# Performance work log

Hardware: AMD Instinct MI355X
Metric: run time of the kernel (lower is better)

The kernel has to match this reference:

```python
import jax, jax.numpy as jnp
import numpy as np

DIM = 1024
NUM_HEADS = 16
HEAD_DIM = DIM // NUM_HEADS
SEQ = 2048
BATCH = 2


def setup_inputs() -> dict:
    key = jax.random.key(0)
    kx, kq, kk, kv, ko, kb = jax.random.split(key, 6)
    s = 0.02
    return {
        "x": jax.random.normal(kx, (BATCH, SEQ, DIM), dtype=jnp.float32),
        "W_q": jax.random.normal(kq, (DIM, DIM), dtype=jnp.float32) * s,
        "W_k": jax.random.normal(kk, (DIM, DIM), dtype=jnp.float32) * s,
        "W_v": jax.random.normal(kv, (DIM, DIM), dtype=jnp.float32) * s,
        "W_o": jax.random.normal(ko, (DIM, DIM), dtype=jnp.float32) * s,
        "b_o": jax.random.normal(kb, (DIM,), dtype=jnp.float32) * s,
    }


def reference(x, W_q, W_k, W_v, W_o, b_o):
    b, n, d = x.shape
    # Linear layers (torch Linear: y = x @ W.T); weights here stored as [out, in]
    q = jnp.einsum('bnd,ed->bne', x, W_q).reshape(b, n, NUM_HEADS, HEAD_DIM)
    k = jnp.einsum('bnd,ed->bne', x, W_k).reshape(b, n, NUM_HEADS, HEAD_DIM)
    v = jnp.einsum('bnd,ed->bne', x, W_v).reshape(b, n, NUM_HEADS, HEAD_DIM)
    # scores: [b, h, q, k]
    scores = jnp.einsum('bqhd,bkhd->bhqk', q, k)
    causal = jnp.tril(jnp.ones((n, n), dtype=bool))  # True = keep
    scores = jnp.where(causal, scores, -jnp.inf)
    weights = jax.nn.softmax(scores / jnp.sqrt(jnp.float32(HEAD_DIM)), axis=-1)
    ctx = jnp.einsum('bhqk,bkhd->bqhd', weights, v).reshape(b, n, d)
    return jnp.einsum('bnd,ed->bne', ctx, W_o) + b_o
```

## Files before the change

### kernel.cpp

```cpp
#include <hip/hip_runtime.h>
#include <hip/hip_bf16.h>

#define DIM 1024
#define NHEADS 16
#define HD 64
#define SEQ 2048
#define BATCH 2
#define MROWS (BATCH * SEQ)
#define MB (1024u * 1024u)
#define NT (SEQ / 64)

typedef __bf16 bf16x8 __attribute__((ext_vector_type(8)));
typedef float f32x4 __attribute__((ext_vector_type(4)));
typedef short short8 __attribute__((ext_vector_type(8)));

#define SCQ (0.125f * 1.44269504f)

__device__ __forceinline__ unsigned short f2bf(float f) {
    union { float f; unsigned u; } v; v.f = f;
    unsigned r = v.u + 0x7fffu + ((v.u >> 16) & 1u);
    return (unsigned short)(r >> 16);
}
__device__ __forceinline__ unsigned cvtpk(float lo, float hi) {
    unsigned r;
    asm("v_cvt_pk_bf16_f32 %0, %1, %2" : "=v"(r) : "v"(lo), "v"(hi));
    return r;
}

__device__ __forceinline__ void gld16(const unsigned short* g, unsigned short* l) {
    __builtin_amdgcn_global_load_lds(
        (const __attribute__((address_space(1))) void*)g,
        (__attribute__((address_space(3))) void*)l, 16, 0, 0);
}

#define VWAIT(n) asm volatile("s_waitcnt vmcnt(" #n ")" ::: "memory")
#define BARRIER  do { __builtin_amdgcn_s_barrier(); __builtin_amdgcn_sched_barrier(0); } while (0)

__global__ __launch_bounds__(256) void f2b_kernel(const float* __restrict__ in,
                                                  unsigned short* __restrict__ out,
                                                  int n4) {
    int i = blockIdx.x * 256 + threadIdx.x;
    if (i < n4) {
        float4 v = ((const float4*)in)[i];
        ushort4 o;
        o.x = f2bf(v.x); o.y = f2bf(v.y); o.z = f2bf(v.z); o.w = f2bf(v.w);
        ((ushort4*)out)[i] = o;
    }
}

__global__ __launch_bounds__(256) void f2bw_kernel(
    const float* __restrict__ w0, const float* __restrict__ w1,
    const float* __restrict__ w2, const float* __restrict__ w3,
    unsigned short* __restrict__ o0, unsigned short* __restrict__ o1,
    unsigned short* __restrict__ o2, unsigned short* __restrict__ o3,
    int n4) {
    const float* in; unsigned short* out;
    switch (blockIdx.y) {
        case 0: in = w0; out = o0; break;
        case 1: in = w1; out = o1; break;
        case 2: in = w2; out = o2; break;
        default: in = w3; out = o3; break;
    }
    int i = blockIdx.x * 256 + threadIdx.x;
    if (i < n4) {
        float4 v = ((const float4*)in)[i];
        ushort4 o;
        o.x = f2bf(v.x); o.y = f2bf(v.y); o.z = f2bf(v.z); o.w = f2bf(v.w);
        ((ushort4*)out)[i] = o;
    }
}


#define GEMM_VARS(Aptr, Bptr)                                                  \
    __shared__ unsigned short As[3][128 * 32];                                 \
    __shared__ unsigned short Bs[3][128 * 32];                                 \
    const int tid  = threadIdx.x;                                              \
    const int lane = tid & 63;                                                 \
    const int wid  = tid >> 6;                                                 \
    const int wrow = wid >> 1, wcol = wid & 1;                                 \
    const int l15  = lane & 15;                                                \
    const int lhi  = lane >> 4;                                                \
    f32x4 acc[4][4] = {};                                                      \
    const int r0s = tid >> 2;                                                  \
    const int c0s = (tid & 3) ^ ((r0s >> 1) & 3);                              \
    const int r1s = (tid + 256) >> 2;                                          \
    const int c1s = (tid & 3) ^ ((r1s >> 1) & 3);                              \
    const unsigned short* gA0 = (Aptr) + (size_t)(row0 + r0s) * DIM + c0s * 8; \
    const unsigned short* gA1 = (Aptr) + (size_t)(row0 + r1s) * DIM + c1s * 8; \
    const unsigned short* gB0 = (Bptr) + (size_t)(col0 + r0s) * DIM + c0s * 8; \
    const unsigned short* gB1 = (Bptr) + (size_t)(col0 + r1s) * DIM + c1s * 8;

#define GEMM_STAGE(bi, kofs)                                                   \
    gld16(gA0 + (kofs), &As[bi][tid * 8]);                                     \
    gld16(gA1 + (kofs), &As[bi][(tid + 256) * 8]);                             \
    gld16(gB0 + (kofs), &Bs[bi][tid * 8]);                                     \
    gld16(gB1 + (kofs), &Bs[bi][(tid + 256) * 8]);

#define GEMM_COMPUTE(bi)                                                       \
    {   const unsigned short* Ac = &As[bi][0];                                 \
        const unsigned short* Bc = &Bs[bi][0];                                 \
        bf16x8 af[4], bfr[4];                                                  \
        _Pragma("unroll")                                                      \
        for (int m = 0; m < 4; m++) {                                          \
            int r = wrow * 64 + m * 16 + l15;                                  \
            int c = lhi ^ ((r >> 1) & 3);                                      \
            af[m] = *(const bf16x8*)&Ac[r * 32 + c * 8];                       \
        }                                                                      \
        _Pragma("unroll")                                                      \
        for (int n = 0; n < 4; n++) {                                          \
            int r = wcol * 64 + n * 16 + l15;                                  \
            int c = lhi ^ ((r >> 1) & 3);                                      \
            bfr[n] = *(const bf16x8*)&Bc[r * 32 + c * 8];                      \
        }                                                                      \
        __builtin_amdgcn_s_setprio(1);                                         \
        _Pragma("unroll")                                                      \
        for (int m = 0; m < 4; m++)                                            \
            _Pragma("unroll")                                                  \
            for (int n = 0; n < 4; n++)                                        \
                acc[m][n] = __builtin_amdgcn_mfma_f32_16x16x32_bf16(           \
                    af[m], bfr[n], acc[m][n], 0, 0, 0);                        \
        __builtin_amdgcn_s_setprio(0);                                         \
    }

#define GEMM_PIPELINE()                                                        \
    GEMM_STAGE(0, 0)                                                           \
    GEMM_STAGE(1, 32)                                                          \
    int bi = 0;                                                                \
    for (int k0 = 0; k0 + 96 <= DIM; k0 += 32) {                               \
        VWAIT(4);                                                              \
        BARRIER;                                                               \
        int b2 = bi + 2; if (b2 >= 3) b2 -= 3;                                 \
        GEMM_STAGE(b2, k0 + 64)                                                \
        GEMM_COMPUTE(bi)                                                       \
        bi = (bi + 1 == 3) ? 0 : bi + 1;                                       \
    }                                                                          \
    VWAIT(4);                                                                  \
    BARRIER;                                                                   \
    GEMM_COMPUTE(bi)                                                           \
    bi = (bi + 1 == 3) ? 0 : bi + 1;                                           \
    VWAIT(0);                                                                  \
    BARRIER;                                                                   \
    GEMM_COMPUTE(bi)

__global__ __launch_bounds__(256) void qkv_gemm(
    const unsigned short* __restrict__ A,
    const unsigned short* __restrict__ Wqb,
    const unsigned short* __restrict__ Wkb,
    const unsigned short* __restrict__ Wvb,
    unsigned short* __restrict__ Qb,
    unsigned short* __restrict__ Kbf,
    unsigned short* __restrict__ Vtb)
{
    const int lb  = ((int)blockIdx.x & 7) * 96 + ((int)blockIdx.x >> 3);
    const int xx  = lb % 24;
    const int yy  = lb / 24;
    const int sel = xx >> 3;
    const unsigned short* Bw = (sel == 0) ? Wqb : ((sel == 1) ? Wkb : Wvb);
    const int row0 = yy * 128;
    const int col0 = (xx & 7) * 128;

    GEMM_VARS(A, Bw)
    GEMM_PIPELINE()

    const int cr = lhi * 4;
    unsigned short* outRM = (sel == 0) ? Qb : Kbf;
    #pragma unroll
    for (int m = 0; m < 4; m++) {
        #pragma unroll
        for (int n = 0; n < 4; n++) {
            #pragma unroll
            for (int j = 0; j < 4; j++) {
                int gr = row0 + wrow * 64 + m * 16 + cr + j;
                int gc = col0 + wcol * 64 + n * 16 + l15;
                float v = acc[m][n][j];
                if (sel == 0) v *= SCQ;
                unsigned short hv = f2bf(v);
                if (sel < 2) {
                    outRM[(size_t)gr * DIM + gc] = hv;
                } else {
                    int bb = gr >> 11, s = gr & 2047;
                    int hh = gc >> 6,  d = gc & 63;
                    Vtb[(((size_t)bb * NHEADS + hh) * HD + d) * SEQ + s] = hv;
                }
            }
        }
    }
}

__global__ __launch_bounds__(256) void o_gemm(
    const unsigned short* __restrict__ A,
    const unsigned short* __restrict__ Bw,
    float* __restrict__ Cp,
    const float* __restrict__ bias)
{
    const int lb  = ((int)blockIdx.x & 7) * 32 + ((int)blockIdx.x >> 3);
    const int xx  = lb % 8;
    const int yy  = lb / 8;
    const int row0 = yy * 128;
    const int col0 = xx * 128;

    GEMM_VARS(A, Bw)
    GEMM_PIPELINE()

    const int cr = lhi * 4;
    #pragma unroll
    for (int m = 0; m < 4; m++) {
        #pragma unroll
        for (int n = 0; n < 4; n++) {
            #pragma unroll
            for (int j = 0; j < 4; j++) {
                int gr = row0 + wrow * 64 + m * 16 + cr + j;
                int gc = col0 + wcol * 64 + n * 16 + l15;
                Cp[(size_t)gr * DIM + gc] = acc[m][n][j] + bias[gc];
            }
        }
    }
}

#define ATTN_COMPUTE(bi, t)                                                    \
    {   const unsigned short* Kc = &Ks[bi][0];                                 \
        const unsigned short* Vc = &Vs[bi][0];                                 \
        f32x4 sacc[4] = {};                                                    \
        __builtin_amdgcn_s_setprio(1);                                         \
        _Pragma("unroll")                                                      \
        for (int ks = 0; ks < 2; ++ks) {                                       \
            bf16x8 bq = ks ? aq1 : aq0;                                        \
            _Pragma("unroll")                                                  \
            for (int nt = 0; nt < 4; nt++) {                                   \
                int r = nt * 16 + l15;                                         \
                int c = (ks * 4 + lhi) ^ (r & 7);                              \
                bf16x8 ak = *(const bf16x8*)&Kc[r * 64 + c * 8];               \
                sacc[nt] = __builtin_amdgcn_mfma_f32_16x16x32_bf16(            \
                    ak, bq, sacc[nt], 0, 0, 0);                                \
            }                                                                  \
        }                                                                      \
        __builtin_amdgcn_s_setprio(0);                                         \
        const bool diag = ((t) == qblk);                                       \
        _Pragma("unroll")                                                      \
        for (int nt = 0; nt < 4; nt++) {                                       \
            float pv[4];                                                       \
            _Pragma("unroll")                                                  \
            for (int j = 0; j < 4; j++) {                                      \
                bool msk = diag && (nt * 16 + lhi * 4 + j > (w & 3) * 16 + l15); \
                pv[j] = msk ? 0.f : exp2f(sacc[nt][j]);                        \
            }                                                                  \
            *(uint2*)&Ps[w][l15][nt * 16 + lhi * 4] =                          \
                make_uint2(cvtpk(pv[0], pv[1]), cvtpk(pv[2], pv[3]));          \
        }                                                                      \
        __builtin_amdgcn_s_setprio(1);                                         \
        _Pragma("unroll")                                                      \
        for (int ks = 0; ks < 2; ++ks) {                                       \
            bf16x8 ap = *(const bf16x8*)&Ps[w][l15][ks * 32 + lhi * 8];        \
            _Pragma("unroll")                                                  \
            for (int dt = 0; dt < 4; dt++) {                                   \
                int r = dt * 16 + l15;                                         \
                int c = (ks * 4 + lhi) ^ (r & 7);                              \
                bf16x8 bv = *(const bf16x8*)&Vc[r * 64 + c * 8];               \
                octx[dt] = __builtin_amdgcn_mfma_f32_16x16x32_bf16(            \
                    ap, bv, octx[dt], 0, 0, 0);                                \
            }                                                                  \
            octxS = __builtin_amdgcn_mfma_f32_16x16x32_bf16(ap, vones, octxS, 0, 0, 0); \
        }                                                                      \
        __builtin_amdgcn_s_setprio(0);                                         \
    }

__global__ __launch_bounds__(512) void attn_kernel(
    const unsigned short* __restrict__ Q,
    const unsigned short* __restrict__ Kb,
    const unsigned short* __restrict__ Vt,
    unsigned short* __restrict__ Ctx)
{
    __shared__ unsigned short Ks[3][64 * 64];
    __shared__ unsigned short Vs[3][64 * 64];
    __shared__ unsigned short Ps[8][16][72];

    const int tid  = threadIdx.x;
    const int lane = tid & 63;
    const int w    = tid >> 6;
    const int lb   = ((int)blockIdx.x & 7) * 64 + ((int)blockIdx.x >> 3);
    const int pair = lb & 15;
    const int h    = (lb >> 4) & 15;
    const int b    = lb >> 8;
    const int l15  = lane & 15;
    const int lhi  = lane >> 4;

    const int qblk   = (w < 4) ? pair : (NT - 1 - pair);
    const int qw     = qblk * 64 + (w & 3) * 16;
    const int ntiles = NT - pair;

    const size_t qrow = ((size_t)b * SEQ + qw + l15) * DIM + h * HD;
    bf16x8 aq0 = *(const bf16x8*)(Q + qrow + lhi * 8);
    bf16x8 aq1 = *(const bf16x8*)(Q + qrow + 32 + lhi * 8);

    const int srow = tid >> 3;
    const int sc16 = (tid & 7) ^ (srow & 7);
    const unsigned short* gK = Kb + ((size_t)b * SEQ + srow) * DIM + h * HD + sc16 * 8;
    const unsigned short* gV = Vt + (((size_t)b * NHEADS + h) * HD + srow) * SEQ + sc16 * 8;

    bf16x8 vones;
    #pragma unroll
    for (int i = 0; i < 8; i++) vones[i] = (__bf16)1.0f;

    f32x4 octx[4] = {};
    f32x4 octxS = {};

    gld16(gK,                  &Ks[0][tid * 8]);
    gld16(gV,                  &Vs[0][tid * 8]);
    gld16(gK + (size_t)64 * DIM, &Ks[1][tid * 8]);
    gld16(gV + 64,             &Vs[1][tid * 8]);

    int bi = 0;
    for (int t = 0; t < ntiles; ++t) {
        if (t < ntiles - 1) { VWAIT(2); } else { VWAIT(0); }
        BARRIER;
        if (t + 2 < ntiles) {
            int b2 = bi + 2; if (b2 >= 3) b2 -= 3;
            gld16(gK + (size_t)(t + 2) * 64 * DIM, &Ks[b2][tid * 8]);
            gld16(gV + (size_t)(t + 2) * 64,       &Vs[b2][tid * 8]);
        }
        if (t <= qblk) ATTN_COMPUTE(bi, t);
        bi = (bi + 1 == 3) ? 0 : bi + 1;
    }

    #pragma unroll
    for (int j = 0; j < 4; j++) {
        float inv = 1.0f / octxS[j];
        #pragma unroll
        for (int dt = 0; dt < 4; dt++) {
            Ctx[((size_t)b * SEQ + qw + lhi * 4 + j) * DIM + h * HD + dt * 16 + l15] =
                f2bf(octx[dt][j] * inv);
        }
    }
}

extern "C" void kernel_launch(void* const* d_in, const int* in_sizes, int n_in,
                              void* d_out, int out_size, void* d_ws, size_t ws_size,
                              hipStream_t stream) {
    const float* x  = (const float*)d_in[0];
    const float* Wq = (const float*)d_in[1];
    const float* Wk = (const float*)d_in[2];
    const float* Wv = (const float*)d_in[3];
    const float* Wo = (const float*)d_in[4];
    const float* bo = (const float*)d_in[5];

    char* ws = (char*)d_ws;
    unsigned short* xb   = (unsigned short*)(ws + 0 * MB);
    unsigned short* Wqb  = (unsigned short*)(ws + 8 * MB);
    unsigned short* Wkb  = (unsigned short*)(ws + 10 * MB);
    unsigned short* Wvb  = (unsigned short*)(ws + 12 * MB);
    unsigned short* Wob  = (unsigned short*)(ws + 14 * MB);
    unsigned short* Qb   = (unsigned short*)(ws + 16 * MB);
    unsigned short* Kbf  = (unsigned short*)(ws + 24 * MB);
    unsigned short* Vtb  = (unsigned short*)(ws + 32 * MB);
    unsigned short* ctxb = (unsigned short*)(ws + 40 * MB);

    f2b_kernel<<<4096, 256, 0, stream>>>(x, xb, (MROWS * DIM) / 4);
    f2bw_kernel<<<dim3(1024, 4), 256, 0, stream>>>(Wq, Wk, Wv, Wo, Wqb, Wkb, Wvb, Wob, (DIM * DIM) / 4);

    qkv_gemm<<<768, 256, 0, stream>>>(xb, Wqb, Wkb, Wvb, Qb, Kbf, Vtb);

    attn_kernel<<<512, 512, 0, stream>>>(Qb, Kbf, Vtb, ctxb);

    o_gemm<<<256, 256, 0, stream>>>(ctxb, Wob, (float*)d_out, bo);
}
```

Baseline: 121.9 us.

## Enlarge QKV GEMM tiles to 256x256 with 512 threads and split-phase pipeline

The QKV projection GEMM moves from 128x128 tiles with 256 threads to 256x256 tiles with 512 threads (8 waves, each computing 128x64). Each K step is split into two halves with interleaved A/B prefetch and extra barriers, so more reuse comes from each LDS load. The aim is less global and LDS traffic per flop. The grid drops to 192 blocks, which is fewer than the CU count and so risks underusing the GPU, and the extra barriers add sync cost. The o_gemm kernel is inlined unchanged, except that it no longer uses setprio.

```diff
diff --git a/kernel.cpp b/kernel.cpp
--- a/kernel.cpp
+++ b/kernel.cpp
@@ -70,79 +70,7 @@
     }
 }
 
-
-#define GEMM_VARS(Aptr, Bptr)                                                  \
-    __shared__ unsigned short As[3][128 * 32];                                 \
-    __shared__ unsigned short Bs[3][128 * 32];                                 \
-    const int tid  = threadIdx.x;                                              \
-    const int lane = tid & 63;                                                 \
-    const int wid  = tid >> 6;                                                 \
-    const int wrow = wid >> 1, wcol = wid & 1;                                 \
-    const int l15  = lane & 15;                                                \
-    const int lhi  = lane >> 4;                                                \
-    f32x4 acc[4][4] = {};                                                      \
-    const int r0s = tid >> 2;                                                  \
-    const int c0s = (tid & 3) ^ ((r0s >> 1) & 3);                              \
-    const int r1s = (tid + 256) >> 2;                                          \
-    const int c1s = (tid & 3) ^ ((r1s >> 1) & 3);                              \
-    const unsigned short* gA0 = (Aptr) + (size_t)(row0 + r0s) * DIM + c0s * 8; \
-    const unsigned short* gA1 = (Aptr) + (size_t)(row0 + r1s) * DIM + c1s * 8; \
-    const unsigned short* gB0 = (Bptr) + (size_t)(col0 + r0s) * DIM + c0s * 8; \
-    const unsigned short* gB1 = (Bptr) + (size_t)(col0 + r1s) * DIM + c1s * 8;
-
-#define GEMM_STAGE(bi, kofs)                                                   \
-    gld16(gA0 + (kofs), &As[bi][tid * 8]);                                     \
-    gld16(gA1 + (kofs), &As[bi][(tid + 256) * 8]);                             \
-    gld16(gB0 + (kofs), &Bs[bi][tid * 8]);                                     \
-    gld16(gB1 + (kofs), &Bs[bi][(tid + 256) * 8]);
-
-#define GEMM_COMPUTE(bi)                                                       \
-    {   const unsigned short* Ac = &As[bi][0];                                 \
-        const unsigned short* Bc = &Bs[bi][0];                                 \
-        bf16x8 af[4], bfr[4];                                                  \
-        _Pragma("unroll")                                                      \
-        for (int m = 0; m < 4; m++) {                                          \
-            int r = wrow * 64 + m * 16 + l15;                                  \
-            int c = lhi ^ ((r >> 1) & 3);                                      \
-            af[m] = *(const bf16x8*)&Ac[r * 32 + c * 8];                       \
-        }                                                                      \
-        _Pragma("unroll")                                                      \
-        for (int n = 0; n < 4; n++) {                                          \
-            int r = wcol * 64 + n * 16 + l15;                                  \
-            int c = lhi ^ ((r >> 1) & 3);                                      \
-            bfr[n] = *(const bf16x8*)&Bc[r * 32 + c * 8];                      \
-        }                                                                      \
-        __builtin_amdgcn_s_setprio(1);                                         \
-        _Pragma("unroll")                                                      \
-        for (int m = 0; m < 4; m++)                                            \
-            _Pragma("unroll")                                                  \
-            for (int n = 0; n < 4; n++)                                        \
-                acc[m][n] = __builtin_amdgcn_mfma_f32_16x16x32_bf16(           \
-                    af[m], bfr[n], acc[m][n], 0, 0, 0);                        \
-        __builtin_amdgcn_s_setprio(0);                                         \
-    }
-
-#define GEMM_PIPELINE()                                                        \
-    GEMM_STAGE(0, 0)                                                           \
-    GEMM_STAGE(1, 32)                                                          \
-    int bi = 0;                                                                \
-    for (int k0 = 0; k0 + 96 <= DIM; k0 += 32) {                               \
-        VWAIT(4);                                                              \
-        BARRIER;                                                               \
-        int b2 = bi + 2; if (b2 >= 3) b2 -= 3;                                 \
-        GEMM_STAGE(b2, k0 + 64)                                                \
-        GEMM_COMPUTE(bi)                                                       \
-        bi = (bi + 1 == 3) ? 0 : bi + 1;                                       \
-    }                                                                          \
-    VWAIT(4);                                                                  \
-    BARRIER;                                                                   \
-    GEMM_COMPUTE(bi)                                                           \
-    bi = (bi + 1 == 3) ? 0 : bi + 1;                                           \
-    VWAIT(0);                                                                  \
-    BARRIER;                                                                   \
-    GEMM_COMPUTE(bi)
-
-__global__ __launch_bounds__(256) void qkv_gemm(
+__global__ __launch_bounds__(512) void qkv_gemm(
     const unsigned short* __restrict__ A,
     const unsigned short* __restrict__ Wqb,
     const unsigned short* __restrict__ Wkb,
@@ -151,27 +79,103 @@
     unsigned short* __restrict__ Kbf,
     unsigned short* __restrict__ Vtb)
 {
-    const int lb  = ((int)blockIdx.x & 7) * 96 + ((int)blockIdx.x >> 3);
-    const int xx  = lb % 24;
-    const int yy  = lb / 24;
-    const int sel = xx >> 3;
+    __shared__ unsigned short As[3][256 * 32];
+    __shared__ unsigned short Bs[3][256 * 32];
+
+    const int tid  = threadIdx.x;
+    const int lane = tid & 63;
+    const int w    = tid >> 6;
+    const int wr   = w >> 2;
+    const int wc   = w & 3;
+    const int l15  = lane & 15;
+    const int lhi  = lane >> 4;
+
+    const int lb   = ((int)blockIdx.x & 7) * 24 + ((int)blockIdx.x >> 3);
+    const int yy   = lb & 15;
+    const int xx   = lb >> 4;
+    const int sel  = xx >> 2;
     const unsigned short* Bw = (sel == 0) ? Wqb : ((sel == 1) ? Wkb : Wvb);
-    const int row0 = yy * 128;
-    const int col0 = (xx & 7) * 128;
-
-    GEMM_VARS(A, Bw)
-    GEMM_PIPELINE()
+    const int row0 = yy * 256;
+    const int col0 = (xx & 3) * 256;
+
+    const int srow   = tid >> 2;
+    const int schunk = (tid & 3) ^ (srow & 3);
+    const unsigned short* gA  = A  + (size_t)(row0 + srow)       * DIM + schunk * 8;
+    const unsigned short* gA2 = A  + (size_t)(row0 + 128 + srow) * DIM + schunk * 8;
+    const unsigned short* gB  = Bw + (size_t)(col0 + srow)       * DIM + schunk * 8;
+    const unsigned short* gB2 = Bw + (size_t)(col0 + 128 + srow) * DIM + schunk * 8;
+
+#define STAGE_A(bi, k0) { gld16(gA + (k0), &As[bi][tid * 8]); gld16(gA2 + (k0), &As[bi][(tid + 512) * 8]); }
+#define STAGE_B(bi, k0) { gld16(gB + (k0), &Bs[bi][tid * 8]); gld16(gB2 + (k0), &Bs[bi][(tid + 512) * 8]); }
+
+    f32x4 acc[8][4] = {};
+
+    const int arow = wr * 128 + l15;
+    const int brow = wc * 64 + l15;
+    const int fpos = (lhi ^ (l15 & 3)) * 8;
+
+    STAGE_A(0, 0)  STAGE_B(0, 0)
+    STAGE_A(1, 32) STAGE_B(1, 32)
+    VWAIT(4);
+    BARRIER;
+
+    int bi = 0;
+    for (int t = 0; t < 32; ++t) {
+        const unsigned short* Ac = &As[bi][0];
+        const unsigned short* Bc = &Bs[bi][0];
+        int b2 = bi + 2; if (b2 >= 3) b2 -= 3;
+        const int k2 = (t + 2) * 32;
+        const bool pf = (t < 30);
+
+        bf16x8 af[4], bfr[4];
+        #pragma unroll
+        for (int m = 0; m < 4; m++)
+            af[m] = *(const bf16x8*)&Ac[(arow + m * 16) * 32 + fpos];
+        #pragma unroll
+        for (int n = 0; n < 4; n++)
+            bfr[n] = *(const bf16x8*)&Bc[(brow + n * 16) * 32 + fpos];
+        if (pf) STAGE_A(b2, k2)
+        BARRIER;
+        __builtin_amdgcn_s_setprio(1);
+        #pragma unroll
+        for (int m = 0; m < 4; m++)
+            #pragma unroll
+            for (int n = 0; n < 4; n++)
+                acc[m][n] = __builtin_amdgcn_mfma_f32_16x16x32_bf16(af[m], bfr[n], acc[m][n], 0, 0, 0);
+        __builtin_amdgcn_s_setprio(0);
+        BARRIER;
+
+        bf16x8 ag[4];
+        #pragma unroll
+        for (int m = 0; m < 4; m++)
+            ag[m] = *(const bf16x8*)&Ac[(arow + (m + 4) * 16) * 32 + fpos];
+        if (pf) STAGE_B(b2, k2)
+        if (pf) { VWAIT(4); } else { VWAIT(0); }
+        BARRIER;
+        __builtin_amdgcn_s_setprio(1);
+        #pragma unroll
+        for (int m = 0; m < 4; m++)
+            #pragma unroll
+            for (int n = 0; n < 4; n++)
+                acc[m + 4][n] = __builtin_amdgcn_mfma_f32_16x16x32_bf16(ag[m], bfr[n], acc[m + 4][n], 0, 0, 0);
+        __builtin_amdgcn_s_setprio(0);
+        BARRIER;
+
+        bi = (bi + 1 == 3) ? 0 : bi + 1;
+    }
+#undef STAGE_A
+#undef STAGE_B
 
     const int cr = lhi * 4;
     unsigned short* outRM = (sel == 0) ? Qb : Kbf;
     #pragma unroll
-    for (int m = 0; m < 4; m++) {
+    for (int m = 0; m < 8; m++) {
         #pragma unroll
         for (int n = 0; n < 4; n++) {
             #pragma unroll
             for (int j = 0; j < 4; j++) {
-                int gr = row0 + wrow * 64 + m * 16 + cr + j;
-                int gc = col0 + wcol * 64 + n * 16 + l15;
+                int gr = row0 + wr * 128 + m * 16 + cr + j;
+                int gc = col0 + wc * 64 + n * 16 + l15;
                 float v = acc[m][n][j];
                 if (sel == 0) v *= SCQ;
                 unsigned short hv = f2bf(v);
@@ -193,14 +197,81 @@
     float* __restrict__ Cp,
     const float* __restrict__ bias)
 {
+    __shared__ unsigned short As[3][128 * 32];
+    __shared__ unsigned short Bs[3][128 * 32];
+
     const int lb  = ((int)blockIdx.x & 7) * 32 + ((int)blockIdx.x >> 3);
     const int xx  = lb % 8;
     const int yy  = lb / 8;
     const int row0 = yy * 128;
     const int col0 = xx * 128;
 
-    GEMM_VARS(A, Bw)
-    GEMM_PIPELINE()
+    const int tid  = threadIdx.x;
+    const int lane = tid & 63;
+    const int wid  = tid >> 6;
+    const int wrow = wid >> 1, wcol = wid & 1;
+    const int l15  = lane & 15;
+    const int lhi  = lane >> 4;
+    f32x4 acc[4][4] = {};
+    const int r0s = tid >> 2;
+    const int c0s = (tid & 3) ^ ((r0s >> 1) & 3);
+    const int r1s = (tid + 256) >> 2;
+    const int c1s = (tid & 3) ^ ((r1s >> 1) & 3);
+    const unsigned short* gA0 = A  + (size_t)(row0 + r0s) * DIM + c0s * 8;
+    const unsigned short* gA1 = A  + (size_t)(row0 + r1s) * DIM + c1s * 8;
+    const unsigned short* gB0 = Bw + (size_t)(col0 + r0s) * DIM + c0s * 8;
+    const unsigned short* gB1 = Bw + (size_t)(col0 + r1s) * DIM + c1s * 8;
+
+#define OSTAGE(bi, kofs)                                     \
+    gld16(gA0 + (kofs), &As[bi][tid * 8]);                   \
+    gld16(gA1 + (kofs), &As[bi][(tid + 256) * 8]);           \
+    gld16(gB0 + (kofs), &Bs[bi][tid * 8]);                   \
+    gld16(gB1 + (kofs), &Bs[bi][(tid + 256) * 8]);
+
+#define OCOMPUTE(bi)                                                           \
+    {   const unsigned short* Ac = &As[bi][0];                                 \
+        const unsigned short* Bc = &Bs[bi][0];                                 \
+        bf16x8 af[4], bfr[4];                                                  \
+        _Pragma("unroll")                                                      \
+        for (int m = 0; m < 4; m++) {                                          \
+            int r = wrow * 64 + m * 16 + l15;                                  \
+            int c = lhi ^ ((r >> 1) & 3);                                      \
+            af[m] = *(const bf16x8*)&Ac[r * 32 + c * 8];                       \
+        }                                                                      \
+        _Pragma("unroll")                                                      \
+        for (int n = 0; n < 4; n++) {                                          \
+            int r = wcol * 64 + n * 16 + l15;                                  \
+            int c = lhi ^ ((r >> 1) & 3);                                      \
+            bfr[n] = *(const bf16x8*)&Bc[r * 32 + c * 8];                      \
+        }                                                                      \
+        _Pragma("unroll")                                                      \
+        for (int m = 0; m < 4; m++)                                            \
+            _Pragma("unroll")                                                  \
+            for (int n = 0; n < 4; n++)                                        \
+                acc[m][n] = __builtin_amdgcn_mfma_f32_16x16x32_bf16(           \
+                    af[m], bfr[n], acc[m][n], 0, 0, 0);                        \
+    }
+
+    OSTAGE(0, 0)
+    OSTAGE(1, 32)
+    int bi = 0;
+    for (int k0 = 0; k0 + 96 <= DIM; k0 += 32) {
+        VWAIT(4);
+        BARRIER;
+        int b2 = bi + 2; if (b2 >= 3) b2 -= 3;
+        OSTAGE(b2, k0 + 64)
+        OCOMPUTE(bi)
+        bi = (bi + 1 == 3) ? 0 : bi + 1;
+    }
+    VWAIT(4);
+    BARRIER;
+    OCOMPUTE(bi)
+    bi = (bi + 1 == 3) ? 0 : bi + 1;
+    VWAIT(0);
+    BARRIER;
+    OCOMPUTE(bi)
+#undef OSTAGE
+#undef OCOMPUTE
 
     const int cr = lhi * 4;
     #pragma unroll
@@ -304,10 +375,10 @@
     f32x4 octx[4] = {};
     f32x4 octxS = {};
 
-    gld16(gK,                  &Ks[0][tid * 8]);
-    gld16(gV,                  &Vs[0][tid * 8]);
+    gld16(gK,                    &Ks[0][tid * 8]);
+    gld16(gV,                    &Vs[0][tid * 8]);
     gld16(gK + (size_t)64 * DIM, &Ks[1][tid * 8]);
-    gld16(gV + 64,             &Vs[1][tid * 8]);
+    gld16(gV + 64,               &Vs[1][tid * 8]);
 
     int bi = 0;
     for (int t = 0; t < ntiles; ++t) {
@@ -357,7 +428,7 @@
     f2b_kernel<<<4096, 256, 0, stream>>>(x, xb, (MROWS * DIM) / 4);
     f2bw_kernel<<<dim3(1024, 4), 256, 0, stream>>>(Wq, Wk, Wv, Wo, Wqb, Wkb, Wvb, Wob, (DIM * DIM) / 4);
 
-    qkv_gemm<<<768, 256, 0, stream>>>(xb, Wqb, Wkb, Wvb, Qb, Kbf, Vtb);
+    qkv_gemm<<<192, 512, 0, stream>>>(xb, Wqb, Wkb, Wvb, Qb, Kbf, Vtb);
 
     attn_kernel<<<512, 512, 0, stream>>>(Qb, Kbf, Vtb, ctxb);
 
```

Result: slower. 141.6 us (+16.2%).

## Pair adjacent causal query blocks per workgroup and merge conversion kernels

Applied to the files above, without the earlier changes.

The attention grid now gives each workgroup two adjacent query blocks (2p, 2p+1), so both halves share the same key/value tiles, instead of pairing a short and a long block for balance. Blocks are ordered so the longest workloads launch first. Separately, the input and weight fp32-to-bf16 conversions are merged into one launch with a 5-row grid to save a kernel launch. The trade-off is uneven per-workgroup work that relies on heavy-first scheduling for balance, plus many idle threadblocks in the weight rows of the merged conversion grid.

```diff
diff --git a/kernel.cpp b/kernel.cpp
--- a/kernel.cpp
+++ b/kernel.cpp
@@ -36,30 +36,21 @@
 #define VWAIT(n) asm volatile("s_waitcnt vmcnt(" #n ")" ::: "memory")
 #define BARRIER  do { __builtin_amdgcn_s_barrier(); __builtin_amdgcn_sched_barrier(0); } while (0)
 
-__global__ __launch_bounds__(256) void f2b_kernel(const float* __restrict__ in,
-                                                  unsigned short* __restrict__ out,
-                                                  int n4) {
-    int i = blockIdx.x * 256 + threadIdx.x;
-    if (i < n4) {
-        float4 v = ((const float4*)in)[i];
-        ushort4 o;
-        o.x = f2bf(v.x); o.y = f2bf(v.y); o.z = f2bf(v.z); o.w = f2bf(v.w);
-        ((ushort4*)out)[i] = o;
-    }
-}
-
-__global__ __launch_bounds__(256) void f2bw_kernel(
+__global__ __launch_bounds__(256) void f2all_kernel(
+    const float* __restrict__ x,
     const float* __restrict__ w0, const float* __restrict__ w1,
     const float* __restrict__ w2, const float* __restrict__ w3,
+    unsigned short* __restrict__ xb,
     unsigned short* __restrict__ o0, unsigned short* __restrict__ o1,
-    unsigned short* __restrict__ o2, unsigned short* __restrict__ o3,
-    int n4) {
-    const float* in; unsigned short* out;
+    unsigned short* __restrict__ o2, unsigned short* __restrict__ o3)
+{
+    const float* in; unsigned short* out; int n4;
     switch (blockIdx.y) {
-        case 0: in = w0; out = o0; break;
-        case 1: in = w1; out = o1; break;
-        case 2: in = w2; out = o2; break;
-        default: in = w3; out = o3; break;
+        case 0: in = x;  out = xb; n4 = (MROWS * DIM) / 4; break;
+        case 1: in = w0; out = o0; n4 = (DIM * DIM) / 4;   break;
+        case 2: in = w1; out = o1; n4 = (DIM * DIM) / 4;   break;
+        case 3: in = w2; out = o2; n4 = (DIM * DIM) / 4;   break;
+        default: in = w3; out = o3; n4 = (DIM * DIM) / 4;  break;
     }
     int i = blockIdx.x * 256 + threadIdx.x;
     if (i < n4) {
@@ -277,16 +268,19 @@
     const int tid  = threadIdx.x;
     const int lane = tid & 63;
     const int w    = tid >> 6;
-    const int lb   = ((int)blockIdx.x & 7) * 64 + ((int)blockIdx.x >> 3);
-    const int pair = lb & 15;
-    const int h    = (lb >> 4) & 15;
-    const int b    = lb >> 8;
+    const int bid  = (int)blockIdx.x;
+    const int half = bid >> 8;
+    const int idx  = bid & 255;
+    const int h    = idx & 15;
+    const int b    = (idx >> 4) & 1;
+    const int slot = idx >> 5;
+    const int p    = half ? slot : (15 - slot);
     const int l15  = lane & 15;
     const int lhi  = lane >> 4;
 
-    const int qblk   = (w < 4) ? pair : (NT - 1 - pair);
+    const int qblk   = 2 * p + (w >> 2);
     const int qw     = qblk * 64 + (w & 3) * 16;
-    const int ntiles = NT - pair;
+    const int ntiles = 2 * p + 2;
 
     const size_t qrow = ((size_t)b * SEQ + qw + l15) * DIM + h * HD;
     bf16x8 aq0 = *(const bf16x8*)(Q + qrow + lhi * 8);
@@ -304,10 +298,10 @@
     f32x4 octx[4] = {};
     f32x4 octxS = {};
 
-    gld16(gK,                  &Ks[0][tid * 8]);
-    gld16(gV,                  &Vs[0][tid * 8]);
+    gld16(gK,                    &Ks[0][tid * 8]);
+    gld16(gV,                    &Vs[0][tid * 8]);
     gld16(gK + (size_t)64 * DIM, &Ks[1][tid * 8]);
-    gld16(gV + 64,             &Vs[1][tid * 8]);
+    gld16(gV + 64,               &Vs[1][tid * 8]);
 
     int bi = 0;
     for (int t = 0; t < ntiles; ++t) {
@@ -354,8 +348,8 @@
     unsigned short* Vtb  = (unsigned short*)(ws + 32 * MB);
     unsigned short* ctxb = (unsigned short*)(ws + 40 * MB);
 
-    f2b_kernel<<<4096, 256, 0, stream>>>(x, xb, (MROWS * DIM) / 4);
-    f2bw_kernel<<<dim3(1024, 4), 256, 0, stream>>>(Wq, Wk, Wv, Wo, Wqb, Wkb, Wvb, Wob, (DIM * DIM) / 4);
+    f2all_kernel<<<dim3(4096, 5), 256, 0, stream>>>(x, Wq, Wk, Wv, Wo,
+                                                    xb, Wqb, Wkb, Wvb, Wob);
 
     qkv_gemm<<<768, 256, 0, stream>>>(xb, Wqb, Wkb, Wvb, Qb, Kbf, Vtb);
 
```

Measured after the change: 122.7 us. Within noise of the previous version (+0.7%).
